# Kernel tuning notes

Measured on AMD Instinct MI355X. Metric: run time of the kernel, lower is better.

The kernel has to match this reference:

```python
import jax, jax.numpy as jnp
import numpy as np

B, C, H, W = 64, 256, 32, 32
S, D, ITERS = 8, 256, 3
EPS = 1e-5


def _ln(x, g, b):
    mu = jnp.mean(x, axis=-1, keepdims=True)
    var = jnp.var(x, axis=-1, keepdims=True)
    return (x - mu) * jax.lax.rsqrt(var + EPS) * g + b


def setup_inputs() -> dict:
    key = jax.random.key(0)
    ks = jax.random.split(key, 12)
    s = 0.02
    return {
        "x": jax.random.normal(ks[0], (B, C, H, W), dtype=jnp.float32),
        "slots_mu": jax.random.normal(ks[1], (1, S, D), dtype=jnp.float32),
        "ln_in_g": jnp.ones((C,), jnp.float32), "ln_in_b": jnp.zeros((C,), jnp.float32),
        "wk": jax.random.normal(ks[2], (D, C), jnp.float32) * s,
        "wv": jax.random.normal(ks[3], (D, C), jnp.float32) * s,
        "ln_s_g": jnp.ones((D,), jnp.float32), "ln_s_b": jnp.zeros((D,), jnp.float32),
        "wq": jax.random.normal(ks[4], (D, D), jnp.float32) * s,
        "gru_wih": jax.random.normal(ks[5], (3 * D, D), jnp.float32) * s,
        "gru_whh": jax.random.normal(ks[6], (3 * D, D), jnp.float32) * s,
        "gru_bih": jnp.zeros((3 * D,), jnp.float32),
        "gru_bhh": jnp.zeros((3 * D,), jnp.float32),
        "ln_m_g": jnp.ones((D,), jnp.float32), "ln_m_b": jnp.zeros((D,), jnp.float32),
        "mlp_w1": jax.random.normal(ks[7], (D, D), jnp.float32) * s,
        "mlp_b1": jnp.zeros((D,), jnp.float32),
        "mlp_w2": jax.random.normal(ks[8], (D, D), jnp.float32) * s,
        "mlp_b2": jnp.zeros((D,), jnp.float32),
    }


def _gru_cell(x, h, wih, whh, bih, bhh):
    # PyTorch GRUCell math. x, h: [BS, D]
    gi = x @ wih.T + bih  # [BS, 3D]
    gh = h @ whh.T + bhh
    ir, iz, inn = jnp.split(gi, 3, axis=-1)
    hr, hz, hn = jnp.split(gh, 3, axis=-1)
    r = jax.nn.sigmoid(ir + hr)
    z = jax.nn.sigmoid(iz + hz)
    n = jnp.tanh(inn + r * hn)
    return (1.0 - z) * n + z * h


def reference(x, slots_mu, ln_in_g, ln_in_b, wk, wv, ln_s_g, ln_s_b, wq,
              gru_wih, gru_whh, gru_bih, gru_bhh, ln_m_g, ln_m_b,
              mlp_w1, mlp_b1, mlp_w2, mlp_b2):
    b, c, h, w = x.shape
    n = h * w
    scale = jnp.asarray(D, x.dtype) ** -0.5
    x_flat = jnp.transpose(x.reshape(b, c, n), (0, 2, 1))  # [B, N, C]
    x_norm = _ln(x_flat, ln_in_g, ln_in_b)
    k = x_norm @ wk.T  # [B, N, D]
    v = x_norm @ wv.T  # [B, N, D]
    slots = jnp.broadcast_to(slots_mu, (b, S, D))
    attn = None
    for _ in range(ITERS):
        q = _ln(slots, ln_s_g, ln_s_b) @ wq.T  # [B, S, D]
        logits = jnp.einsum('bnd,bsd->bns', k, q) * scale
        attn = jax.nn.softmax(logits, axis=-1)  # softmax over SLOTS
        updates = jnp.einsum('bns,bnd->bsd', attn, v)
        slots = _gru_cell(updates.reshape(-1, D), slots.reshape(-1, D),
                          gru_wih, gru_whh, gru_bih, gru_bhh).reshape(b, S, D)
        hmid = jax.nn.relu(_ln(slots, ln_m_g, ln_m_b) @ mlp_w1.T + mlp_b1)
        slots = slots + (hmid @ mlp_w2.T + mlp_b2)
    return slots, attn
```

## Files before the change

kernel.cpp:

```cpp
#include <hip/hip_runtime.h>

#define NPIX 1024
#define CIN  256
#define EPSV 1e-5f
#define SP 264
#define AP 72
#define BKA 264

typedef __attribute__((ext_vector_type(8))) short bf16x8;
typedef __attribute__((ext_vector_type(4))) float f32x4;

__device__ __forceinline__ short f2bf(float f) {
  unsigned u = __float_as_uint(f);
  unsigned r = (u + 0x7FFFu + ((u >> 16) & 1u)) >> 16;
  return (short)r;
}
__device__ __forceinline__ float b2f(short s) {
  return __uint_as_float(((unsigned)(unsigned short)s) << 16);
}

__global__ __launch_bounds__(256) void wcvt(
    const float* __restrict__ wq, const float* __restrict__ wih,
    const float* __restrict__ whh, const float* __restrict__ w1,
    const float* __restrict__ w2,
    short* __restrict__ wq_b, short* __restrict__ wih_b, short* __restrict__ whh_b,
    short* __restrict__ w1_b, short* __restrict__ w2_b) {
  int id = blockIdx.x * 256 + threadIdx.x;
  if      (id <  65536) wq_b [id         ] = f2bf(wq [id         ]);
  else if (id < 262144) wih_b[id -  65536] = f2bf(wih[id -  65536]);
  else if (id < 458752) whh_b[id - 262144] = f2bf(whh[id - 262144]);
  else if (id < 524288) w1_b [id - 458752] = f2bf(w1 [id - 458752]);
  else if (id < 589824) w2_b [id - 524288] = f2bf(w2 [id - 524288]);
}

__global__ __launch_bounds__(256) void wfold(
    const float* __restrict__ wk, const float* __restrict__ wv,
    const float* __restrict__ g, const float* __restrict__ bet,
    short* __restrict__ wkv_b, float* __restrict__ kvA, float* __restrict__ kvB) {
  __shared__ float ra[4], rb[4];
  int d = blockIdx.x;
  int t = threadIdx.x;
  const float* wrow = (d < 256) ? (wk + (size_t)d * 256) : (wv + (size_t)(d - 256) * 256);
  float w = wrow[t], gg = g[t], bb = bet[t];
  float pa = gg * w, pb = bb * w;
  wkv_b[(size_t)d * 256 + t] = f2bf(pa);
  #pragma unroll
  for (int m = 1; m < 64; m <<= 1) { pa += __shfl_xor(pa, m); pb += __shfl_xor(pb, m); }
  int wave = t >> 6, lane = t & 63;
  if (lane == 0) { ra[wave] = pa; rb[wave] = pb; }
  __syncthreads();
  if (t == 0) {
    kvA[d] = ra[0] + ra[1] + ra[2] + ra[3];
    kvB[d] = rb[0] + rb[1] + rb[2] + rb[3];
  }
}

__global__ __launch_bounds__(256) void xt_stats(
    const float* __restrict__ x, short* __restrict__ xT,
    float* __restrict__ mu, float* __restrict__ rstd) {
  __shared__ float ps[2][128], pq[2][128];
  int t = threadIdx.x;
  int pt = blockIdx.x & 7, b = blockIdx.x >> 3;
  int n0 = pt << 7;
  int q = t >> 2, j = t & 3;
  int pql = q & 31;
  int chal = t >> 7;
  int p0 = n0 + (pql << 2);
  const float* xb = x + (size_t)b * CIN * NPIX;
  short* xrow = xT + (size_t)((b << 10) + p0 + j) * 256;
  float s = 0.f, sq = 0.f;
  #pragma unroll
  for (int i = 0; i < 16; i++) {
    bf16x8 o;
    #pragma unroll
    for (int sub = 0; sub < 2; sub++) {
      int c0 = (i << 4) + (chal << 3) + (sub << 2);
      float4 v = *(const float4*)(xb + (size_t)(c0 + j) * NPIX + p0);
      float v0 = v.x, v1 = v.y, v2 = v.z, v3 = v.w;
      float e0 = __shfl_xor((j & 1) ? v0 : v1, 1);
      float e1 = __shfl_xor((j & 1) ? v2 : v3, 1);
      if (j & 1) { v0 = e0; v2 = e1; } else { v1 = e0; v3 = e1; }
      float e2 = __shfl_xor((j & 2) ? v0 : v2, 2);
      float e3 = __shfl_xor((j & 2) ? v1 : v3, 2);
      if (j & 2) { v0 = e2; v1 = e3; } else { v2 = e2; v3 = e3; }
      s += v0 + v1 + v2 + v3;
      sq += v0 * v0 + v1 * v1 + v2 * v2 + v3 * v3;
      o[(sub << 2) + 0] = f2bf(v0);
      o[(sub << 2) + 1] = f2bf(v1);
      o[(sub << 2) + 2] = f2bf(v2);
      o[(sub << 2) + 3] = f2bf(v3);
    }
    *(bf16x8*)(xrow + (i << 4) + (chal << 3)) = o;
  }
  ps[chal][t & 127] = s;
  pq[chal][t & 127] = sq;
  __syncthreads();
  if (t < 128) {
    float ss = ps[0][t] + ps[1][t];
    float qq = pq[0][t] + pq[1][t];
    float m = ss * (1.f / 256.f);
    float var = qq * (1.f / 256.f) - m * m;
    int p = (b << 10) + n0 + t;
    mu[p] = m;
    rstd[p] = rsqrtf(var + EPSV);
  }
}

__global__ __launch_bounds__(256, 2) void kv_gemm(
    const short* __restrict__ xT,
    const float* __restrict__ mu, const float* __restrict__ rstd,
    const short* __restrict__ wkv,
    const float* __restrict__ kvA, const float* __restrict__ kvB,
    short* __restrict__ kout, short* __restrict__ vTout) {
  __shared__ __align__(16) short As[128 * BKA];
  __shared__ float mus[128], rss[128];
  int t = threadIdx.x;
  int pt = blockIdx.x & 7, b = blockIdx.x >> 3;
  int n0 = pt << 7;
  const short* xtb = xT + (size_t)((b << 10) + n0) * 256;
  #pragma unroll
  for (int pass = 0; pass < 16; pass++) {
    int idx = (pass << 8) + t;
    int p = idx >> 5, c8 = (idx & 31) << 3;
    bf16x8 v = *(const bf16x8*)(xtb + ((size_t)idx << 3));
    *(bf16x8*)&As[p * BKA + c8] = v;
  }
  if (t < 128) {
    mus[t] = mu[(b << 10) + n0 + t];
    rss[t] = rstd[(b << 10) + n0 + t];
  }
  __syncthreads();
  int w = t >> 6, lane = t & 63, quad = lane >> 4, lid = lane & 15;
  int wm = w & 1, wn = w >> 1;
  #pragma unroll
  for (int nt = 0; nt < 4; nt++) {
    f32x4 acc[4][4];
    #pragma unroll
    for (int i = 0; i < 4; i++)
      #pragma unroll
      for (int j = 0; j < 4; j++) acc[i][j] = 0.f;
    #pragma unroll
    for (int ks = 0; ks < 8; ks++) {
      int kof = (ks << 5) + (quad << 3);
      bf16x8 af[4], bfr[4];
      #pragma unroll
      for (int i = 0; i < 4; i++)
        af[i] = *(const bf16x8*)&As[(wm * 64 + i * 16 + lid) * BKA + kof];
      #pragma unroll
      for (int j = 0; j < 4; j++)
        bfr[j] = *(const bf16x8*)(wkv + (size_t)((nt << 7) + wn * 64 + j * 16 + lid) * 256 + kof);
      #pragma unroll
      for (int i = 0; i < 4; i++)
        #pragma unroll
        for (int j = 0; j < 4; j++)
          acc[i][j] = __builtin_amdgcn_mfma_f32_16x16x32_bf16(af[i], bfr[j], acc[i][j], 0, 0, 0);
    }
    #pragma unroll
    for (int i = 0; i < 4; i++) {
      int pl = wm * 64 + i * 16 + (quad << 2);
      #pragma unroll
      for (int j = 0; j < 4; j++) {
        int dim = (nt << 7) + wn * 64 + j * 16 + lid;
        float Ad = kvA[dim], Bd = kvB[dim];
        if (nt < 2) {
          #pragma unroll
          for (int r = 0; r < 4; r++) {
            float val = rss[pl + r] * (acc[i][j][r] - mus[pl + r] * Ad) + Bd;
            kout[((size_t)((b << 10) + n0 + pl + r)) * 256 + dim] = f2bf(val);
          }
        } else {
          short4 hv;
          hv.x = f2bf(rss[pl + 0] * (acc[i][j][0] - mus[pl + 0] * Ad) + Bd);
          hv.y = f2bf(rss[pl + 1] * (acc[i][j][1] - mus[pl + 1] * Ad) + Bd);
          hv.z = f2bf(rss[pl + 2] * (acc[i][j][2] - mus[pl + 2] * Ad) + Bd);
          hv.w = f2bf(rss[pl + 3] * (acc[i][j][3] - mus[pl + 3] * Ad) + Bd);
          *(short4*)(vTout + (size_t)b * 262144 + (size_t)(dim - 256) * 1024 + n0 + pl) = hv;
        }
      }
    }
  }
}

__global__ __launch_bounds__(256) void slot_init(
    const float* __restrict__ slots_mu,
    const float* __restrict__ lsg, const float* __restrict__ lsb,
    const short* __restrict__ wq_b,
    float* __restrict__ slbuf, short* __restrict__ slbG, short* __restrict__ qb) {
  __shared__ float sl[8][256];
  __shared__ float mus[8], rss[8];
  __shared__ __align__(16) short slnb[8 * SP];
  int b = blockIdx.x, t = threadIdx.x;
  int wave = t >> 6, lane = t & 63, quad = lane >> 4, lid = lane & 15;
  int arow = (lid & 7) * SP, kof0 = quad << 3;
  for (int idx = t; idx < 2048; idx += 256) {
    float v = slots_mu[idx];
    sl[idx >> 8][idx & 255] = v;
    slbuf[(b << 11) + idx] = v;
    slbG[(b << 11) + idx] = f2bf(v);
  }
  __syncthreads();
  {
    int s0 = (wave << 1) + (lane >> 5);
    int l32 = lane & 31;
    float a0 = 0.f, a1 = 0.f;
    #pragma unroll
    for (int j = 0; j < 8; j++) { float v = sl[s0][l32 + (j << 5)]; a0 += v; a1 += v * v; }
    #pragma unroll
    for (int m = 1; m < 32; m <<= 1) { a0 += __shfl_xor(a0, m); a1 += __shfl_xor(a1, m); }
    if (l32 == 0) {
      float mn = a0 * (1.f / 256.f);
      float var = a1 * (1.f / 256.f) - mn * mn;
      mus[s0] = mn; rss[s0] = rsqrtf(var + EPSV);
    }
  }
  __syncthreads();
  for (int idx = t; idx < 2048; idx += 256) {
    int s = idx >> 8, c = idx & 255;
    slnb[s * SP + c] = f2bf((sl[s][c] - mus[s]) * rss[s] * lsg[c] + lsb[c]);
  }
  __syncthreads();
  #pragma unroll
  for (int nt = 0; nt < 4; nt++) {
    int d = (wave << 6) + (nt << 4) + lid;
    f32x4 qa = 0.f;
    #pragma unroll
    for (int ks = 0; ks < 8; ks++) {
      bf16x8 a = *(const bf16x8*)&slnb[arow + (ks << 5) + kof0];
      bf16x8 bb = *(const bf16x8*)(wq_b + (size_t)d * 256 + (ks << 5) + kof0);
      qa = __builtin_amdgcn_mfma_f32_16x16x32_bf16(a, bb, qa, 0, 0, 0);
    }
    #pragma unroll
    for (int r = 0; r < 4; r++) {
      int s = (quad << 2) + r;
      if (s < 8) qb[(b << 11) + (s << 8) + d] = f2bf(qa[r]);
    }
  }
}

__global__ __launch_bounds__(256) void attn_heavy(
    const short* __restrict__ kbuf, const short* __restrict__ vT,
    const short* __restrict__ qb,
    short* __restrict__ partials, float* __restrict__ out_attn, int write_attn) {
  __shared__ __align__(16) short attT[8 * AP];
  int chunk = blockIdx.x, b = blockIdx.y;
  int t = threadIdx.x, wave = t >> 6, lane = t & 63, quad = lane >> 4, lid = lane & 15;
  int kof0 = quad << 3;
  bf16x8 qf[8];
  const short* qpb = qb + ((size_t)b << 11) + (lid & 7) * 256 + kof0;
  #pragma unroll
  for (int ks = 0; ks < 8; ks++) qf[ks] = *(const bf16x8*)(qpb + (ks << 5));
  {
    int p0l = wave << 4;
    const short* kb = kbuf + ((size_t)((b << 10) + (chunk << 6) + p0l + lid)) * 256 + kof0;
    f32x4 la = 0.f;
    #pragma unroll
    for (int ks = 0; ks < 8; ks++) {
      bf16x8 a = *(const bf16x8*)(kb + (ks << 5));
      la = __builtin_amdgcn_mfma_f32_16x16x32_bf16(a, qf[ks], la, 0, 0, 0);
    }
    #pragma unroll
    for (int r = 0; r < 4; r++) {
      float lg = la[r] * 0.0625f;
      float mx = lg;
      #pragma unroll
      for (int m = 1; m < 16; m <<= 1) mx = fmaxf(mx, __shfl_xor(mx, m));
      float e = __expf(lg - mx);
      float sm = e;
      #pragma unroll
      for (int m = 1; m < 16; m <<= 1) sm += __shfl_xor(sm, m);
      float at = (e + e) / sm;
      if (lid < 8) {
        int pl = p0l + (quad << 2) + r;
        attT[lid * AP + pl] = f2bf(at);
        if (write_attn) {
          int p = (chunk << 6) + pl;
          out_attn[((size_t)b << 13) + (p << 3) + lid] = at;
        }
      }
    }
  }
  __syncthreads();
  #pragma unroll
  for (int nt = 0; nt < 4; nt++) {
    int d0 = (wave << 6) + (nt << 4);
    f32x4 ua = 0.f;
    #pragma unroll
    for (int ks = 0; ks < 2; ks++) {
      bf16x8 a = *(const bf16x8*)&attT[(lid & 7) * AP + (ks << 5) + kof0];
      bf16x8 bb = *(const bf16x8*)(vT + (size_t)b * 262144 + (size_t)(d0 + lid) * 1024
                                   + (chunk << 6) + (ks << 5) + kof0);
      ua = __builtin_amdgcn_mfma_f32_16x16x32_bf16(a, bb, ua, 0, 0, 0);
    }
    #pragma unroll
    for (int r = 0; r < 4; r++) {
      int s = (quad << 2) + r;
      if (s < 8)
        partials[(((size_t)(b << 4) + chunk) << 11) + (s << 8) + d0 + lid] = f2bf(ua[r]);
    }
  }
}

__global__ __launch_bounds__(256) void slot_reduce(
    const short* __restrict__ partials,
    float* __restrict__ slbuf, short* __restrict__ slbG, short* __restrict__ qb,
    const short* __restrict__ wih_b, const short* __restrict__ whh_b,
    const float* __restrict__ bih, const float* __restrict__ bhh,
    const float* __restrict__ lmg, const float* __restrict__ lmb,
    const short* __restrict__ w1_b, const float* __restrict__ b1,
    const short* __restrict__ w2_b, const float* __restrict__ b2,
    const float* __restrict__ lsg, const float* __restrict__ lsb,
    const short* __restrict__ wq_b,
    float* __restrict__ out, int last) {
  __shared__ float sl[8][256];
  __shared__ float mus[8], rss[8];
  __shared__ __align__(16) short updb[8 * SP], slb_l[8 * SP], lnmb[8 * SP],
                                  hmb[8 * SP], slnb[8 * SP];
  int b = blockIdx.x, t = threadIdx.x;
  int wave = t >> 6, lane = t & 63, quad = lane >> 4, lid = lane & 15;
  int arow = (lid & 7) * SP, kof0 = quad << 3;
  for (int idx = t; idx < 2048; idx += 256) {
    float sum = 0.f;
    #pragma unroll
    for (int c = 0; c < 16; c++) sum += b2f(partials[(((size_t)(b << 4) + c) << 11) + idx]);
    int s = idx >> 8, dd = idx & 255;
    updb[s * SP + dd] = f2bf(sum);
    sl[s][dd] = slbuf[(b << 11) + idx];
    slb_l[s * SP + dd] = slbG[(b << 11) + idx];
  }
  __syncthreads();
  #pragma unroll
  for (int nt = 0; nt < 4; nt++) {
    int d = (wave << 6) + (nt << 4) + lid;
    f32x4 gi[3], gh[3];
    #pragma unroll
    for (int g = 0; g < 3; g++) { gi[g] = 0.f; gh[g] = 0.f; }
    #pragma unroll
    for (int ks = 0; ks < 8; ks++) {
      bf16x8 au  = *(const bf16x8*)&updb [arow + (ks << 5) + kof0];
      bf16x8 as2 = *(const bf16x8*)&slb_l[arow + (ks << 5) + kof0];
      #pragma unroll
      for (int g = 0; g < 3; g++) {
        bf16x8 bi = *(const bf16x8*)(wih_b + (size_t)((g << 8) + d) * 256 + (ks << 5) + kof0);
        bf16x8 bh = *(const bf16x8*)(whh_b + (size_t)((g << 8) + d) * 256 + (ks << 5) + kof0);
        gi[g] = __builtin_amdgcn_mfma_f32_16x16x32_bf16(au,  bi, gi[g], 0, 0, 0);
        gh[g] = __builtin_amdgcn_mfma_f32_16x16x32_bf16(as2, bh, gh[g], 0, 0, 0);
      }
    }
    float bi0 = bih[d], bi1 = bih[256 + d], bi2 = bih[512 + d];
    float bh0 = bhh[d], bh1 = bhh[256 + d], bh2 = bhh[512 + d];
    #pragma unroll
    for (int r = 0; r < 4; r++) {
      int s = (quad << 2) + r;
      if (s < 8) {
        float rg = 1.f / (1.f + __expf(-(gi[0][r] + bi0 + gh[0][r] + bh0)));
        float zg = 1.f / (1.f + __expf(-(gi[1][r] + bi1 + gh[1][r] + bh1)));
        float ng = tanhf(gi[2][r] + bi2 + rg * (gh[2][r] + bh2));
        sl[s][d] = (1.f - zg) * ng + zg * sl[s][d];
      }
    }
  }
  __syncthreads();
  {
    int s0 = (wave << 1) + (lane >> 5);
    int l32 = lane & 31;
    float a0 = 0.f, a1 = 0.f;
    #pragma unroll
    for (int j = 0; j < 8; j++) { float v = sl[s0][l32 + (j << 5)]; a0 += v; a1 += v * v; }
    #pragma unroll
    for (int m = 1; m < 32; m <<= 1) { a0 += __shfl_xor(a0, m); a1 += __shfl_xor(a1, m); }
    if (l32 == 0) {
      float mn = a0 * (1.f / 256.f);
      float var = a1 * (1.f / 256.f) - mn * mn;
      mus[s0] = mn; rss[s0] = rsqrtf(var + EPSV);
    }
  }
  __syncthreads();
  for (int idx = t; idx < 2048; idx += 256) {
    int s = idx >> 8, c = idx & 255;
    lnmb[s * SP + c] = f2bf((sl[s][c] - mus[s]) * rss[s] * lmg[c] + lmb[c]);
  }
  __syncthreads();
  #pragma unroll
  for (int nt = 0; nt < 4; nt++) {
    int d = (wave << 6) + (nt << 4) + lid;
    f32x4 ha = 0.f;
    #pragma unroll
    for (int ks = 0; ks < 8; ks++) {
      bf16x8 a = *(const bf16x8*)&lnmb[arow + (ks << 5) + kof0];
      bf16x8 bb = *(const bf16x8*)(w1_b + (size_t)d * 256 + (ks << 5) + kof0);
      ha = __builtin_amdgcn_mfma_f32_16x16x32_bf16(a, bb, ha, 0, 0, 0);
    }
    float bb1 = b1[d];
    #pragma unroll
    for (int r = 0; r < 4; r++) {
      int s = (quad << 2) + r;
      if (s < 8) hmb[s * SP + d] = f2bf(fmaxf(ha[r] + bb1, 0.f));
    }
  }
  __syncthreads();
  #pragma unroll
  for (int nt = 0; nt < 4; nt++) {
    int d = (wave << 6) + (nt << 4) + lid;
    f32x4 oa = 0.f;
    #pragma unroll
    for (int ks = 0; ks < 8; ks++) {
      bf16x8 a = *(const bf16x8*)&hmb[arow + (ks << 5) + kof0];
      bf16x8 bb = *(const bf16x8*)(w2_b + (size_t)d * 256 + (ks << 5) + kof0);
      oa = __builtin_amdgcn_mfma_f32_16x16x32_bf16(a, bb, oa, 0, 0, 0);
    }
    float bb2 = b2[d];
    #pragma unroll
    for (int r = 0; r < 4; r++) {
      int s = (quad << 2) + r;
      if (s < 8) sl[s][d] = sl[s][d] + oa[r] + bb2;
    }
  }
  __syncthreads();
  if (last) {
    for (int idx = t; idx < 2048; idx += 256)
      out[(b << 11) + idx] = sl[idx >> 8][idx & 255];
    return;
  }
  for (int idx = t; idx < 2048; idx += 256) {
    float v = sl[idx >> 8][idx & 255];
    slbuf[(b << 11) + idx] = v;
    slbG[(b << 11) + idx] = f2bf(v);
  }
  {
    int s0 = (wave << 1) + (lane >> 5);
    int l32 = lane & 31;
    float a0 = 0.f, a1 = 0.f;
    #pragma unroll
    for (int j = 0; j < 8; j++) { float v = sl[s0][l32 + (j << 5)]; a0 += v; a1 += v * v; }
    #pragma unroll
    for (int m = 1; m < 32; m <<= 1) { a0 += __shfl_xor(a0, m); a1 += __shfl_xor(a1, m); }
    if (l32 == 0) {
      float mn = a0 * (1.f / 256.f);
      float var = a1 * (1.f / 256.f) - mn * mn;
      mus[s0] = mn; rss[s0] = rsqrtf(var + EPSV);
    }
  }
  __syncthreads();
  for (int idx = t; idx < 2048; idx += 256) {
    int s = idx >> 8, c = idx & 255;
    slnb[s * SP + c] = f2bf((sl[s][c] - mus[s]) * rss[s] * lsg[c] + lsb[c]);
  }
  __syncthreads();
  #pragma unroll
  for (int nt = 0; nt < 4; nt++) {
    int d = (wave << 6) + (nt << 4) + lid;
    f32x4 qa = 0.f;
    #pragma unroll
    for (int ks = 0; ks < 8; ks++) {
      bf16x8 a = *(const bf16x8*)&slnb[arow + (ks << 5) + kof0];
      bf16x8 bb = *(const bf16x8*)(wq_b + (size_t)d * 256 + (ks << 5) + kof0);
      qa = __builtin_amdgcn_mfma_f32_16x16x32_bf16(a, bb, qa, 0, 0, 0);
    }
    #pragma unroll
    for (int r = 0; r < 4; r++) {
      int s = (quad << 2) + r;
      if (s < 8) qb[(b << 11) + (s << 8) + d] = f2bf(qa[r]);
    }
  }
}

extern "C" void kernel_launch(void* const* d_in, const int* in_sizes, int n_in,
                              void* d_out, int out_size, void* d_ws, size_t ws_size,
                              hipStream_t stream) {
  const float* x        = (const float*)d_in[0];
  const float* slots_mu = (const float*)d_in[1];
  const float* ln_in_g  = (const float*)d_in[2];
  const float* ln_in_b  = (const float*)d_in[3];
  const float* wk       = (const float*)d_in[4];
  const float* wv       = (const float*)d_in[5];
  const float* ln_s_g   = (const float*)d_in[6];
  const float* ln_s_b   = (const float*)d_in[7];
  const float* wq       = (const float*)d_in[8];
  const float* wih      = (const float*)d_in[9];
  const float* whh      = (const float*)d_in[10];
  const float* bih      = (const float*)d_in[11];
  const float* bhh      = (const float*)d_in[12];
  const float* lmg      = (const float*)d_in[13];
  const float* lmb      = (const float*)d_in[14];
  const float* w1       = (const float*)d_in[15];
  const float* b1       = (const float*)d_in[16];
  const float* w2       = (const float*)d_in[17];
  const float* b2       = (const float*)d_in[18];
  float* out = (float*)d_out;
  float* out_attn = out + 131072;

  char* ws = (char*)d_ws;
  short* kbuf   = (short*)(ws);
  short* vT     = (short*)(ws + 33554432);
  short* wkv_b  = (short*)(ws + 67108864);
  short* wq_b   = (short*)(ws + 67371008);
  short* wih_b  = (short*)(ws + 67502080);
  short* whh_b  = (short*)(ws + 67895296);
  short* w1_b   = (short*)(ws + 68288512);
  short* w2_b   = (short*)(ws + 68419584);
  float* slbuf  = (float*)(ws + 68550656);
  short* slbG   = (short*)(ws + 69074944);
  short* qb     = (short*)(ws + 69337088);
  short* parts  = (short*)(ws + 69599232);
  float* kvA    = (float*)(ws + 73793536);
  float* kvB    = (float*)(ws + 73795584);
  float* muB    = (float*)(ws + 73797632);
  float* rstdB  = (float*)(ws + 74059776);

  wcvt<<<2304, 256, 0, stream>>>(wq, wih, whh, w1, w2,
                                 wq_b, wih_b, whh_b, w1_b, w2_b);
  wfold<<<512, 256, 0, stream>>>(wk, wv, ln_in_g, ln_in_b, wkv_b, kvA, kvB);
  xt_stats<<<512, 256, 0, stream>>>(x, kbuf, muB, rstdB);
  kv_gemm<<<512, 256, 0, stream>>>(kbuf, muB, rstdB, wkv_b, kvA, kvB, kbuf, vT);
  slot_init<<<64, 256, 0, stream>>>(slots_mu, ln_s_g, ln_s_b, wq_b, slbuf, slbG, qb);
  for (int it = 0; it < 3; it++) {
    attn_heavy<<<dim3(16, 64), 256, 0, stream>>>(kbuf, vT, qb, parts, out_attn,
                                                 (it == 2) ? 1 : 0);
    slot_reduce<<<64, 256, 0, stream>>>(parts, slbuf, slbG, qb,
                                        wih_b, whh_b, bih, bhh, lmg, lmb,
                                        w1_b, b1, w2_b, b2, ln_s_g, ln_s_b, wq_b,
                                        out, (it == 2) ? 1 : 0);
  }
}
```

Measured before the change: 394.7 us.

## Widen slot_reduce to 1024 threads with one 16-column tile per wave

The per-batch slot update kernel now runs 16 waves per block instead of 4. Each wave computes a single 16-column tile of the GRU, MLP and query GEMMs, where before each wave looped over four tiles. The partial-sum reduction and the slot state loads are split across thread groups and vectorised to 8-wide loads. The LayerNorm statistics now use one full wave per slot. The aim is more latency hiding and parallelism in this serial, 64-block kernel, at the cost of higher register pressure from the 1024-thread launch bound.

```diff
diff --git a/kernel.cpp b/kernel.cpp
--- a/kernel.cpp
+++ b/kernel.cpp
@@ -300,7 +300,7 @@
   }
 }
 
-__global__ __launch_bounds__(256) void slot_reduce(
+__global__ __launch_bounds__(1024) void slot_reduce(
     const short* __restrict__ partials,
     float* __restrict__ slbuf, short* __restrict__ slbG, short* __restrict__ qb,
     const short* __restrict__ wih_b, const short* __restrict__ whh_b,
@@ -318,33 +318,55 @@
   int b = blockIdx.x, t = threadIdx.x;
   int wave = t >> 6, lane = t & 63, quad = lane >> 4, lid = lane & 15;
   int arow = (lid & 7) * SP, kof0 = quad << 3;
-  for (int idx = t; idx < 2048; idx += 256) {
-    float sum = 0.f;
-    #pragma unroll
-    for (int c = 0; c < 16; c++) sum += b2f(partials[(((size_t)(b << 4) + c) << 11) + idx]);
-    int s = idx >> 8, dd = idx & 255;
-    updb[s * SP + dd] = f2bf(sum);
-    sl[s][dd] = slbuf[(b << 11) + idx];
-    slb_l[s * SP + dd] = slbG[(b << 11) + idx];
-  }
-  __syncthreads();
-  #pragma unroll
-  for (int nt = 0; nt < 4; nt++) {
-    int d = (wave << 6) + (nt << 4) + lid;
-    f32x4 gi[3], gh[3];
-    #pragma unroll
-    for (int g = 0; g < 3; g++) { gi[g] = 0.f; gh[g] = 0.f; }
-    #pragma unroll
-    for (int ks = 0; ks < 8; ks++) {
-      bf16x8 au  = *(const bf16x8*)&updb [arow + (ks << 5) + kof0];
-      bf16x8 as2 = *(const bf16x8*)&slb_l[arow + (ks << 5) + kof0];
-      #pragma unroll
-      for (int g = 0; g < 3; g++) {
-        bf16x8 bi = *(const bf16x8*)(wih_b + (size_t)((g << 8) + d) * 256 + (ks << 5) + kof0);
-        bf16x8 bh = *(const bf16x8*)(whh_b + (size_t)((g << 8) + d) * 256 + (ks << 5) + kof0);
-        gi[g] = __builtin_amdgcn_mfma_f32_16x16x32_bf16(au,  bi, gi[g], 0, 0, 0);
-        gh[g] = __builtin_amdgcn_mfma_f32_16x16x32_bf16(as2, bh, gh[g], 0, 0, 0);
-      }
+  int d = (wave << 4) + lid;
+  if (t < 256) {
+    int s = t >> 5, d8 = (t & 31) << 3;
+    float acc[8];
+    #pragma unroll
+    for (int i = 0; i < 8; i++) acc[i] = 0.f;
+    #pragma unroll
+    for (int c = 0; c < 16; c++) {
+      bf16x8 v = *(const bf16x8*)(partials + ((((size_t)(b << 4) + c) << 11) + (s << 8) + d8));
+      #pragma unroll
+      for (int i = 0; i < 8; i++) acc[i] += b2f(v[i]);
+    }
+    bf16x8 o;
+    #pragma unroll
+    for (int i = 0; i < 8; i++) o[i] = f2bf(acc[i]);
+    *(bf16x8*)&updb[s * SP + d8] = o;
+  } else if (t < 512) {
+    int tt = t - 256;
+    int s = tt >> 5, d8 = (tt & 31) << 3;
+    bf16x8 v = *(const bf16x8*)(slbG + ((b << 11) + (s << 8) + d8));
+    *(bf16x8*)&slb_l[s * SP + d8] = v;
+  } else if (t < 768) {
+    int tt = t - 512;
+    int s = tt >> 5, d8 = (tt & 31) << 3;
+    float4 v0 = *(const float4*)(slbuf + ((b << 11) + (s << 8) + d8));
+    float4 v1 = *(const float4*)(slbuf + ((b << 11) + (s << 8) + d8 + 4));
+    *(float4*)&sl[s][d8] = v0;
+    *(float4*)&sl[s][d8 + 4] = v1;
+  }
+  __syncthreads();
+  {
+    f32x4 gi0 = 0.f, gi1 = 0.f, gi2 = 0.f, gh0 = 0.f, gh1 = 0.f, gh2 = 0.f;
+    #pragma unroll
+    for (int ks = 0; ks < 8; ks++) {
+      int kof = (ks << 5) + kof0;
+      bf16x8 au = *(const bf16x8*)&updb [arow + kof];
+      bf16x8 ah = *(const bf16x8*)&slb_l[arow + kof];
+      bf16x8 w0 = *(const bf16x8*)(wih_b + (size_t)(0 * 256 + d) * 256 + kof);
+      bf16x8 w1r = *(const bf16x8*)(wih_b + (size_t)(1 * 256 + d) * 256 + kof);
+      bf16x8 w2r = *(const bf16x8*)(wih_b + (size_t)(2 * 256 + d) * 256 + kof);
+      bf16x8 u0 = *(const bf16x8*)(whh_b + (size_t)(0 * 256 + d) * 256 + kof);
+      bf16x8 u1 = *(const bf16x8*)(whh_b + (size_t)(1 * 256 + d) * 256 + kof);
+      bf16x8 u2 = *(const bf16x8*)(whh_b + (size_t)(2 * 256 + d) * 256 + kof);
+      gi0 = __builtin_amdgcn_mfma_f32_16x16x32_bf16(au, w0, gi0, 0, 0, 0);
+      gi1 = __builtin_amdgcn_mfma_f32_16x16x32_bf16(au, w1r, gi1, 0, 0, 0);
+      gi2 = __builtin_amdgcn_mfma_f32_16x16x32_bf16(au, w2r, gi2, 0, 0, 0);
+      gh0 = __builtin_amdgcn_mfma_f32_16x16x32_bf16(ah, u0, gh0, 0, 0, 0);
+      gh1 = __builtin_amdgcn_mfma_f32_16x16x32_bf16(ah, u1, gh1, 0, 0, 0);
+      gh2 = __builtin_amdgcn_mfma_f32_16x16x32_bf16(ah, u2, gh2, 0, 0, 0);
     }
     float bi0 = bih[d], bi1 = bih[256 + d], bi2 = bih[512 + d];
     float bh0 = bhh[d], bh1 = bhh[256 + d], bh2 = bhh[512 + d];
@@ -352,42 +374,39 @@
     for (int r = 0; r < 4; r++) {
       int s = (quad << 2) + r;
       if (s < 8) {
-        float rg = 1.f / (1.f + __expf(-(gi[0][r] + bi0 + gh[0][r] + bh0)));
-        float zg = 1.f / (1.f + __expf(-(gi[1][r] + bi1 + gh[1][r] + bh1)));
-        float ng = tanhf(gi[2][r] + bi2 + rg * (gh[2][r] + bh2));
+        float rg = 1.f / (1.f + __expf(-(gi0[r] + bi0 + gh0[r] + bh0)));
+        float zg = 1.f / (1.f + __expf(-(gi1[r] + bi1 + gh1[r] + bh1)));
+        float ng = tanhf(gi2[r] + bi2 + rg * (gh2[r] + bh2));
         sl[s][d] = (1.f - zg) * ng + zg * sl[s][d];
       }
     }
   }
   __syncthreads();
-  {
-    int s0 = (wave << 1) + (lane >> 5);
-    int l32 = lane & 31;
+  if (wave < 8) {
     float a0 = 0.f, a1 = 0.f;
     #pragma unroll
-    for (int j = 0; j < 8; j++) { float v = sl[s0][l32 + (j << 5)]; a0 += v; a1 += v * v; }
-    #pragma unroll
-    for (int m = 1; m < 32; m <<= 1) { a0 += __shfl_xor(a0, m); a1 += __shfl_xor(a1, m); }
-    if (l32 == 0) {
+    for (int j = 0; j < 4; j++) { float v = sl[wave][lane + (j << 6)]; a0 += v; a1 += v * v; }
+    #pragma unroll
+    for (int m = 1; m < 64; m <<= 1) { a0 += __shfl_xor(a0, m); a1 += __shfl_xor(a1, m); }
+    if (lane == 0) {
       float mn = a0 * (1.f / 256.f);
       float var = a1 * (1.f / 256.f) - mn * mn;
-      mus[s0] = mn; rss[s0] = rsqrtf(var + EPSV);
-    }
-  }
-  __syncthreads();
-  for (int idx = t; idx < 2048; idx += 256) {
+      mus[wave] = mn; rss[wave] = rsqrtf(var + EPSV);
+    }
+  }
+  __syncthreads();
+  for (int idx = t; idx < 2048; idx += 1024) {
     int s = idx >> 8, c = idx & 255;
     lnmb[s * SP + c] = f2bf((sl[s][c] - mus[s]) * rss[s] * lmg[c] + lmb[c]);
   }
   __syncthreads();
-  #pragma unroll
-  for (int nt = 0; nt < 4; nt++) {
-    int d = (wave << 6) + (nt << 4) + lid;
+  {
     f32x4 ha = 0.f;
     #pragma unroll
     for (int ks = 0; ks < 8; ks++) {
-      bf16x8 a = *(const bf16x8*)&lnmb[arow + (ks << 5) + kof0];
-      bf16x8 bb = *(const bf16x8*)(w1_b + (size_t)d * 256 + (ks << 5) + kof0);
+      int kof = (ks << 5) + kof0;
+      bf16x8 a = *(const bf16x8*)&lnmb[arow + kof];
+      bf16x8 bb = *(const bf16x8*)(w1_b + (size_t)d * 256 + kof);
       ha = __builtin_amdgcn_mfma_f32_16x16x32_bf16(a, bb, ha, 0, 0, 0);
     }
     float bb1 = b1[d];
@@ -398,14 +417,13 @@
     }
   }
   __syncthreads();
-  #pragma unroll
-  for (int nt = 0; nt < 4; nt++) {
-    int d = (wave << 6) + (nt << 4) + lid;
+  {
     f32x4 oa = 0.f;
     #pragma unroll
     for (int ks = 0; ks < 8; ks++) {
-      bf16x8 a = *(const bf16x8*)&hmb[arow + (ks << 5) + kof0];
-      bf16x8 bb = *(const bf16x8*)(w2_b + (size_t)d * 256 + (ks << 5) + kof0);
+      int kof = (ks << 5) + kof0;
+      bf16x8 a = *(const bf16x8*)&hmb[arow + kof];
+      bf16x8 bb = *(const bf16x8*)(w2_b + (size_t)d * 256 + kof);
       oa = __builtin_amdgcn_mfma_f32_16x16x32_bf16(a, bb, oa, 0, 0, 0);
     }
     float bb2 = b2[d];
@@ -417,43 +435,40 @@
   }
   __syncthreads();
   if (last) {
-    for (int idx = t; idx < 2048; idx += 256)
+    for (int idx = t; idx < 2048; idx += 1024)
       out[(b << 11) + idx] = sl[idx >> 8][idx & 255];
     return;
   }
-  for (int idx = t; idx < 2048; idx += 256) {
+  for (int idx = t; idx < 2048; idx += 1024) {
     float v = sl[idx >> 8][idx & 255];
     slbuf[(b << 11) + idx] = v;
     slbG[(b << 11) + idx] = f2bf(v);
   }
-  {
-    int s0 = (wave << 1) + (lane >> 5);
-    int l32 = lane & 31;
+  if (wave < 8) {
     float a0 = 0.f, a1 = 0.f;
     #pragma unroll
-    for (int j = 0; j < 8; j++) { float v = sl[s0][l32 + (j << 5)]; a0 += v; a1 += v * v; }
-    #pragma unroll
-    for (int m = 1; m < 32; m <<= 1) { a0 += __shfl_xor(a0, m); a1 += __shfl_xor(a1, m); }
-    if (l32 == 0) {
+    for (int j = 0; j < 4; j++) { float v = sl[wave][lane + (j << 6)]; a0 += v; a1 += v * v; }
+    #pragma unroll
+    for (int m = 1; m < 64; m <<= 1) { a0 += __shfl_xor(a0, m); a1 += __shfl_xor(a1, m); }
+    if (lane == 0) {
       float mn = a0 * (1.f / 256.f);
       float var = a1 * (1.f / 256.f) - mn * mn;
-      mus[s0] = mn; rss[s0] = rsqrtf(var + EPSV);
-    }
-  }
-  __syncthreads();
-  for (int idx = t; idx < 2048; idx += 256) {
+      mus[wave] = mn; rss[wave] = rsqrtf(var + EPSV);
+    }
+  }
+  __syncthreads();
+  for (int idx = t; idx < 2048; idx += 1024) {
     int s = idx >> 8, c = idx & 255;
     slnb[s * SP + c] = f2bf((sl[s][c] - mus[s]) * rss[s] * lsg[c] + lsb[c]);
   }
   __syncthreads();
-  #pragma unroll
-  for (int nt = 0; nt < 4; nt++) {
-    int d = (wave << 6) + (nt << 4) + lid;
+  {
     f32x4 qa = 0.f;
     #pragma unroll
     for (int ks = 0; ks < 8; ks++) {
-      bf16x8 a = *(const bf16x8*)&slnb[arow + (ks << 5) + kof0];
-      bf16x8 bb = *(const bf16x8*)(wq_b + (size_t)d * 256 + (ks << 5) + kof0);
+      int kof = (ks << 5) + kof0;
+      bf16x8 a = *(const bf16x8*)&slnb[arow + kof];
+      bf16x8 bb = *(const bf16x8*)(wq_b + (size_t)d * 256 + kof);
       qa = __builtin_amdgcn_mfma_f32_16x16x32_bf16(a, bb, qa, 0, 0, 0);
     }
     #pragma unroll
@@ -516,9 +531,9 @@
   for (int it = 0; it < 3; it++) {
     attn_heavy<<<dim3(16, 64), 256, 0, stream>>>(kbuf, vT, qb, parts, out_attn,
                                                  (it == 2) ? 1 : 0);
-    slot_reduce<<<64, 256, 0, stream>>>(parts, slbuf, slbG, qb,
-                                        wih_b, whh_b, bih, bhh, lmg, lmb,
-                                        w1_b, b1, w2_b, b2, ln_s_g, ln_s_b, wq_b,
-                                        out, (it == 2) ? 1 : 0);
-  }
-}
+    slot_reduce<<<64, 1024, 0, stream>>>(parts, slbuf, slbG, qb,
+                                         wih_b, whh_b, bih, bhh, lmg, lmb,
+                                         w1_b, b1, w2_b, b2, ln_s_g, ln_s_b, wq_b,
+                                         out, (it == 2) ? 1 : 0);
+  }
+}
```

After: 361.4 us. 8.4% less time.
